# Performance work log

Measured on AMD Instinct MI355X. Metric: run time of the kernel, lower is better.

Reference implementation:

```python
import jax, jax.numpy as jnp
import numpy as np

PQ_M = 8
VALS_PER_DIM = 256
SUB_DIM = 64
EMB = PQ_M * SUB_DIM  # 512
NUM_ITEMS = 1_000_000
BATCH = 256
SEQ = 512


def setup_inputs() -> dict:
    key = jax.random.key(0)
    k1, k2, k3 = jax.random.split(key, 3)
    input_ids = jax.random.randint(k1, (BATCH, SEQ), 0, NUM_ITEMS, dtype=jnp.int64 if jax.config.jax_enable_x64 else jnp.int32).astype(jnp.int32)
    item_codes = jax.random.randint(k2, (NUM_ITEMS, PQ_M), 0, VALS_PER_DIM, dtype=jnp.int32)
    centroids = jax.random.normal(k3, (PQ_M, VALS_PER_DIM, SUB_DIM), dtype=jnp.float32)
    # module zeroes centroid index 0 in every subspace at init
    centroids = centroids.at[:, 0, :].set(0.0)
    return {"input_ids": input_ids, "item_codes": item_codes, "centroids": centroids}


def reference(input_ids, item_codes, centroids):
    # input_ids: [B, S] int; item_codes: [N, M] int32; centroids: [M, V, D] f32
    codes = item_codes[input_ids]                       # [B, S, M]
    codes = jnp.minimum(codes, VALS_PER_DIM - 1)        # clamp per subspace
    byte_idx = jnp.arange(PQ_M, dtype=jnp.int32)        # [M]
    # per-subspace gather: centroids[m, codes[b,s,m]] -> [B, S, M, D]
    sub = centroids[byte_idx[None, None, :], codes]
    B, S = input_ids.shape
    result = sub.reshape(B, S, EMB)                     # concat subspaces
    pad = (input_ids == 0)[:, :, None]                  # zero padding tokens
    return jnp.where(pad, 0.0, result)
```

## Files before the change

kernel.cpp:

```cpp
#include <hip/hip_runtime.h>


#define VALS_ 256
#define NTOK_ (256 * 512)
#define TOKS_BLK 32
#define THREADS 256
#define ITERS 16

typedef float f4 __attribute__((ext_vector_type(4)));

__global__ __launch_bounds__(THREADS) void ItemCode_kernel(
    const int* __restrict__ input_ids,
    const int* __restrict__ item_codes,
    const float* __restrict__ centroids,
    float* __restrict__ out)
{
    const int tid  = threadIdx.x;
    const int wave = tid >> 6;
    const int lane = tid & 63;

    const int tok0w = blockIdx.x * TOKS_BLK + wave * 8;

    const int id = input_ids[tok0w + (lane >> 3)];
    int code = __builtin_nontemporal_load(&item_codes[id * 8 + (lane & 7)]);
    code = min(code, VALS_ - 1);
    code = id ? code : 0;
    const int off = (((lane & 7) << 8) + code) << 4;

    const f4* __restrict__ cent4 = reinterpret_cast<const f4*>(centroids);
    f4* __restrict__ out4 = reinterpret_cast<f4*>(out);
    const int ob = tok0w * 128 + lane;
    const int s4 = lane & 15;

    int ci[ITERS];
    #pragma unroll
    for (int it = 0; it < ITERS; ++it) {
        const int owner = ((it >> 1) << 3) | ((it & 1) << 2) | (lane >> 4);
        ci[it] = __shfl(off, owner) + s4;
    }

    f4 v[ITERS];
    #pragma unroll
    for (int it = 0; it < ITERS; ++it)
        v[it] = cent4[ci[it]];

    #pragma unroll
    for (int it = 0; it < ITERS; ++it)
        __builtin_nontemporal_store(v[it], &out4[ob + it * 64]);
}

extern "C" void kernel_launch(void* const* d_in, const int* in_sizes, int n_in,
                              void* d_out, int out_size, void* d_ws, size_t ws_size,
                              hipStream_t stream) {
    const int*   input_ids  = (const int*)d_in[0];
    const int*   item_codes = (const int*)d_in[1];
    const float* centroids  = (const float*)d_in[2];
    float*       out        = (float*)d_out;

    dim3 grid(NTOK_ / TOKS_BLK), block(THREADS);
    ItemCode_kernel<<<grid, block, 0, stream>>>(input_ids, item_codes, centroids, out);
}
```

Measured before the change: 58.19 us.

## Split random item-code gather into a prepass kernel writing offsets to workspace

Adds a prepass kernel where each thread handles one token, loading its 8 item codes with two 16-byte vector loads, clamping them and writing precomputed centroid offsets to the workspace. A second streaming kernel then reads these offsets contiguously and performs the centroid gather and output store. The aim is to separate the latency-bound random gather from the bandwidth-bound output stream. In exchange it adds a second launch and a 4 MB workspace write and read-back, and it falls back to the fused kernel when the workspace is too small.

Measured after the change: 59.65 us. 1.03x slower.

```diff
diff --git a/kernel.cpp b/kernel.cpp
--- a/kernel.cpp
+++ b/kernel.cpp
@@ -8,24 +8,43 @@
 #define ITERS 16
 
 typedef float f4 __attribute__((ext_vector_type(4)));
+typedef int   i4 __attribute__((ext_vector_type(4)));
 
-__global__ __launch_bounds__(THREADS) void ItemCode_kernel(
+__global__ __launch_bounds__(THREADS) void ItemCode_prepass(
     const int* __restrict__ input_ids,
     const int* __restrict__ item_codes,
+    int* __restrict__ ws_off)
+{
+    const int t  = blockIdx.x * THREADS + threadIdx.x;
+    const int id = input_ids[t];
+    const i4* row = reinterpret_cast<const i4*>(item_codes + (size_t)id * 8);
+    i4 c0 = __builtin_nontemporal_load(&row[0]);
+    i4 c1 = __builtin_nontemporal_load(&row[1]);
+
+    i4 o0, o1;
+    #pragma unroll
+    for (int j = 0; j < 4; ++j) {
+        int cj = min(c0[j], VALS_ - 1); cj = id ? cj : 0;
+        o0[j] = ((j << 8) + cj) << 4;
+        int ck = min(c1[j], VALS_ - 1); ck = id ? ck : 0;
+        o1[j] = (((j + 4) << 8) + ck) << 4;
+    }
+    i4* dst = reinterpret_cast<i4*>(ws_off + (size_t)t * 8);
+    dst[0] = o0;
+    dst[1] = o1;
+}
+
+__global__ __launch_bounds__(THREADS) void ItemCode_stream(
+    const int* __restrict__ ws_off,
     const float* __restrict__ centroids,
     float* __restrict__ out)
 {
     const int tid  = threadIdx.x;
     const int wave = tid >> 6;
     const int lane = tid & 63;
-
     const int tok0w = blockIdx.x * TOKS_BLK + wave * 8;
 
-    const int id = input_ids[tok0w + (lane >> 3)];
-    int code = __builtin_nontemporal_load(&item_codes[id * 8 + (lane & 7)]);
-    code = min(code, VALS_ - 1);
-    code = id ? code : 0;
-    const int off = (((lane & 7) << 8) + code) << 4;
+    const int off = ws_off[tok0w * 8 + lane];
 
     const f4* __restrict__ cent4 = reinterpret_cast<const f4*>(centroids);
     f4* __restrict__ out4 = reinterpret_cast<f4*>(out);
@@ -49,6 +68,43 @@
         __builtin_nontemporal_store(v[it], &out4[ob + it * 64]);
 }
 
+__global__ __launch_bounds__(THREADS) void ItemCode_fused(
+    const int* __restrict__ input_ids,
+    const int* __restrict__ item_codes,
+    const float* __restrict__ centroids,
+    float* __restrict__ out)
+{
+    const int tid  = threadIdx.x;
+    const int wave = tid >> 6;
+    const int lane = tid & 63;
+    const int tok0w = blockIdx.x * TOKS_BLK + wave * 8;
+
+    const int id = input_ids[tok0w + (lane >> 3)];
+    int code = __builtin_nontemporal_load(&item_codes[(size_t)id * 8 + (lane & 7)]);
+    code = min(code, VALS_ - 1);
+    code = id ? code : 0;
+    const int off = (((lane & 7) << 8) + code) << 4;
+
+    const f4* __restrict__ cent4 = reinterpret_cast<const f4*>(centroids);
+    f4* __restrict__ out4 = reinterpret_cast<f4*>(out);
+    const int ob = tok0w * 128 + lane;
+    const int s4 = lane & 15;
+
+    int ci[ITERS];
+    #pragma unroll
+    for (int it = 0; it < ITERS; ++it) {
+        const int owner = ((it >> 1) << 3) | ((it & 1) << 2) | (lane >> 4);
+        ci[it] = __shfl(off, owner) + s4;
+    }
+    f4 v[ITERS];
+    #pragma unroll
+    for (int it = 0; it < ITERS; ++it)
+        v[it] = cent4[ci[it]];
+    #pragma unroll
+    for (int it = 0; it < ITERS; ++it)
+        __builtin_nontemporal_store(v[it], &out4[ob + it * 64]);
+}
+
 extern "C" void kernel_launch(void* const* d_in, const int* in_sizes, int n_in,
                               void* d_out, int out_size, void* d_ws, size_t ws_size,
                               hipStream_t stream) {
@@ -57,6 +113,12 @@
     const float* centroids  = (const float*)d_in[2];
     float*       out        = (float*)d_out;
 
-    dim3 grid(NTOK_ / TOKS_BLK), block(THREADS);
-    ItemCode_kernel<<<grid, block, 0, stream>>>(input_ids, item_codes, centroids, out);
+    const size_t ws_needed = (size_t)NTOK_ * 8 * sizeof(int);
+    if (ws_size >= ws_needed) {
+        int* ws_off = (int*)d_ws;
+        ItemCode_prepass<<<NTOK_ / THREADS, THREADS, 0, stream>>>(input_ids, item_codes, ws_off);
+        ItemCode_stream<<<NTOK_ / TOKS_BLK, THREADS, 0, stream>>>(ws_off, centroids, out);
+    } else {
+        ItemCode_fused<<<NTOK_ / TOKS_BLK, THREADS, 0, stream>>>(input_ids, item_codes, centroids, out);
+    }
 }
```
